# Optimization experiments

Measured on AMD Instinct MI355X. Metric: run time of the kernel, lower is better.

The kernel has to match this reference:

```python
import jax, jax.numpy as jnp
import numpy as np

BN_EPS = 1e-5
K = 3  # k_size


def _unfold(x, k):
    # torch F.unfold with padding=k//2, stride=1, viewed as (B, C, k*k, H, W).
    # Kernel positions are row-major (i slow, j fast), matching torch layout.
    p = k // 2
    B, C, H, W = x.shape
    xp = jnp.pad(x, ((0, 0), (0, 0), (p, p), (p, p)))
    pats = jnp.stack([xp[:, :, i:i + H, j:j + W]
                      for i in range(k) for j in range(k)], axis=2)
    return pats  # (B, C, k*k, H, W)


def _conv1x1(x, w, b):
    # w: (C_out, C_in), x: (B, C_in, H, W)
    return jnp.einsum('oc,bchw->bohw', w, x) + b[None, :, None, None]


def _bn(x, gamma, beta, mean, var):
    inv = gamma / jnp.sqrt(var + BN_EPS)
    return x * inv[None, :, None, None] + (beta - mean * inv)[None, :, None, None]


def setup_inputs() -> dict:
    key = jax.random.key(0)
    ks = jax.random.split(key, 12)
    B, C, H, W = 8, 256, 64, 64
    s = lambda k_, *sh: jax.random.normal(k_, sh, dtype=jnp.float32) * 0.05
    return {
        'x': jax.random.normal(ks[0], (B, C, H, W), dtype=jnp.float32),
        # feature_embedding: Conv2d(C, C, 1) + BN
        'w_embed': s(ks[1], C, C), 'b_embed': jnp.zeros((C,), jnp.float32),
        'bn1_gamma': jnp.ones((C,), jnp.float32), 'bn1_beta': jnp.zeros((C,), jnp.float32),
        'bn1_mean': jnp.zeros((C,), jnp.float32), 'bn1_var': jnp.ones((C,), jnp.float32),
        # enhance: Conv2d(2C, C, 1) + BN
        'w_enh': s(ks[2], C, 2 * C), 'b_enh': jnp.zeros((C,), jnp.float32),
        'bn2_gamma': jnp.ones((C,), jnp.float32), 'bn2_beta': jnp.zeros((C,), jnp.float32),
        'bn2_mean': jnp.zeros((C,), jnp.float32), 'bn2_var': jnp.ones((C,), jnp.float32),
        # weight_gen: Conv2d(2C, C//4, 1) -> ReLU -> Conv2d(C//4, C, 1) -> Sigmoid
        'w_g1': s(ks[3], C // 4, 2 * C), 'b_g1': jnp.zeros((C // 4,), jnp.float32),
        'w_g2': s(ks[4], C, C // 4), 'b_g2': jnp.zeros((C,), jnp.float32),
    }


def reference(x, w_embed, b_embed, bn1_gamma, bn1_beta, bn1_mean, bn1_var,
              w_enh, b_enh, bn2_gamma, bn2_beta, bn2_mean, bn2_var,
              w_g1, b_g1, w_g2, b_g2):
    B, C, H, W = x.shape
    # ---- feature embedding: 1x1 conv + BN (eval) + ReLU
    fe = jax.nn.relu(_bn(_conv1x1(x, w_embed, b_embed),
                         bn1_gamma, bn1_beta, bn1_mean, bn1_var))
    # ---- region similarity: cosine(center pixel, each kxk neighbor) over C
    pats = _unfold(fe, K)                       # (B, C, k2, H, W)
    sim = jnp.einsum('bchw,bckhw->bkhw', fe, pats)
    norm_c = jnp.sqrt(jnp.sum(fe * fe, axis=1))             # (B, H, W)
    norm_p = jnp.sqrt(jnp.sum(pats * pats, axis=1))         # (B, k2, H, W)
    sim = sim / (norm_c[:, None] * norm_p + 1e-7)
    sim = jax.nn.softmax(sim, axis=1)                       # over k2 window
    # ---- dynamic feature aggregation on original x
    xpats = _unfold(x, K)                                   # (B, C, k2, H, W)
    agg = jnp.einsum('bckhw,bkhw->bchw', xpats, sim)
    enhanced = jax.nn.relu(_bn(_conv1x1(jnp.concatenate([x, agg], axis=1), w_enh, b_enh),
                               bn2_gamma, bn2_beta, bn2_mean, bn2_var))
    # ---- output modulation (SE-style gating)
    pooled = jnp.mean(jnp.concatenate([x, enhanced], axis=1), axis=(2, 3), keepdims=True)
    h = jax.nn.relu(_conv1x1(pooled, w_g1, b_g1))
    weights = jax.nn.sigmoid(_conv1x1(h, w_g2, b_g2))       # (B, C, 1, 1)
    return x + weights * enhanced
```

## Files before the change

kernel.cpp:

```cpp
#include <hip/hip_runtime.h>
#include <math.h>

typedef unsigned short u16;
typedef unsigned int   u32;
typedef __attribute__((ext_vector_type(8))) short short8;
typedef __attribute__((ext_vector_type(4))) float f32x4;

#define OFS_XB   0ul
#define OFS_W1B  8388608ul
#define OFS_W2B  8421376ul
#define OFS_B1   8486912ul
#define OFS_B2   8487168ul
#define OFS_POOL 8487424ul
#define OFS_ENH  8491520ul

__device__ __forceinline__ u16 f2bf(float x) {
    union { float f; u32 u; } v; v.f = x;
    u32 r = v.u + 0x7fffu + ((v.u >> 16) & 1u);
    return (u16)(r >> 16);
}
__device__ __forceinline__ float bf2f(u16 h) {
    union { u32 u; float f; } v; v.u = ((u32)h) << 16;
    return v.f;
}
__device__ __forceinline__ void ld_g2l_16(u16* l, const u16* g) {
    __builtin_amdgcn_global_load_lds(
        (const __attribute__((address_space(1))) u32*)g,
        (__attribute__((address_space(3))) u32*)l,
        16, 0, 0);
}

__global__ __launch_bounds__(256) void k_cvt(
    const float* __restrict__ x, u16* __restrict__ xb, float* __restrict__ pool,
    const float* __restrict__ w1, const float* __restrict__ b1,
    const float* __restrict__ g1, const float* __restrict__ be1,
    const float* __restrict__ m1, const float* __restrict__ v1,
    const float* __restrict__ w2, const float* __restrict__ b2,
    const float* __restrict__ g2, const float* __restrict__ be2,
    const float* __restrict__ m2, const float* __restrict__ v2,
    u16* __restrict__ w1b, u16* __restrict__ w2b,
    float* __restrict__ b1f, float* __restrict__ b2f)
{
    __shared__ float tile[64][65];
    const int t = threadIdx.x;
    const int id = blockIdx.x;
    if (id < 1) {
        const float4 z = {0.f, 0.f, 0.f, 0.f};
#pragma unroll
        for (int i = 0; i < 4; ++i) ((float4*)pool)[i * 256 + t] = z;
        return;
    }
    if (id < 771) {
        int idx = (id - 1) * 256 + t;
        if (idx < 65536) {
            int o = idx >> 8;
            float inv = g1[o] * rsqrtf(v1[o] + 1e-5f);
            w1b[idx] = f2bf(w1[idx] * inv);
        } else if (idx < 196608) {
            int j = idx - 65536;
            int o = j >> 9;
            float inv = g2[o] * rsqrtf(v2[o] + 1e-5f);
            w2b[j] = f2bf(w2[j] * inv);
        } else if (idx < 196864) {
            int o = idx - 196608;
            float inv = g1[o] * rsqrtf(v1[o] + 1e-5f);
            b1f[o] = b1[o] * inv + be1[o] - m1[o] * inv;
        } else if (idx < 197120) {
            int o = idx - 196864;
            float inv = g2[o] * rsqrtf(v2[o] + 1e-5f);
            b2f[o] = b2[o] * inv + be2[o] - m2[o] * inv;
        }
        return;
    }
    const int cid = id - 771;
    const int pt = cid & 63, ct = (cid >> 6) & 3, b = cid >> 8;
    const float* src = x + (((size_t)(b * 256 + ct * 64)) << 12) + pt * 64;
#pragma unroll
    for (int i = 0; i < 16; ++i) {
        int idx = i * 256 + t;
        int cl = idx >> 6, pl = idx & 63;
        tile[cl][pl] = src[((size_t)cl << 12) + pl];
    }
    __syncthreads();
#pragma unroll
    for (int i = 0; i < 8; ++i) {
        int idx = i * 256 + t;
        int pl = idx >> 5, c2 = idx & 31;
        int cl = c2 * 2;
        u32 lo = f2bf(tile[cl][pl]);
        u32 hi = f2bf(tile[cl + 1][pl]);
        *(u32*)(xb + (((size_t)(b * 4096 + pt * 64 + pl)) << 9) + ct * 64 + cl) = lo | (hi << 16);
    }
    if (t < 64) {
        float s = 0.f;
#pragma unroll
        for (int i = 0; i < 64; ++i) s += tile[t][i];
        atomicAdd(&pool[(b << 9) + ct * 64 + t], s * (1.f / 4096.f));
    }
}

template<int KIN, bool OUTBF, bool DOPOOL>
__global__ __launch_bounds__(256) void k_gemm(
    const u16* __restrict__ xb, const u16* __restrict__ Wb,
    const float* __restrict__ biasf, void* __restrict__ outp,
    float* __restrict__ poolp)
{
    __shared__ __align__(16) u16 Wl[4096];
    __shared__ __align__(16) u16 Xl[4096];
    __shared__ float sbias[128];
    const int t = threadIdx.x;
    const int lane = t & 63;
    const int wv = t >> 6;
    const int id = blockIdx.x;
    const int p_blk = (((id >> 4) << 3) | (id & 7)) * 128;
    const int o_blk = ((id >> 3) & 1) * 128;
    const int owg = (wv & 1) * 4;
    const int pwg = (wv >> 1) * 4;
    const int r16 = lane & 15, q = lane >> 4;
    if (t < 128) sbias[t] = biasf[o_blk + t];

    f32x4 acc[4][4];
#pragma unroll
    for (int i = 0; i < 4; ++i)
#pragma unroll
        for (int j = 0; j < 4; ++j) acc[i][j] = (f32x4){0.f, 0.f, 0.f, 0.f};

    for (int kc = 0; kc < KIN / 32; ++kc) {
        const int kk = kc * 32 + q * 8;
#pragma unroll
        for (int s = 0; s < 4; ++s) {
            const int bi = wv * 4 + s;
            const u16* g;
            u16* l;
            if (bi < 8) {
                g = Wb + (size_t)(o_blk + bi * 16 + r16) * KIN + kk;
                l = Wl + bi * 512;
            } else {
                g = xb + (((size_t)(p_blk + (bi - 8) * 16 + r16)) << 9) + kk;
                l = Xl + (bi - 8) * 512;
            }
            ld_g2l_16(l, g);
        }
        __syncthreads();
        short8 af[4], bf[4];
#pragma unroll
        for (int i = 0; i < 4; ++i) af[i] = *(const short8*)(Wl + (owg + i) * 512 + lane * 8);
#pragma unroll
        for (int j = 0; j < 4; ++j) bf[j] = *(const short8*)(Xl + (pwg + j) * 512 + lane * 8);
#pragma unroll
        for (int i = 0; i < 4; ++i)
#pragma unroll
            for (int j = 0; j < 4; ++j)
                acc[i][j] = __builtin_amdgcn_mfma_f32_16x16x32_bf16(af[i], bf[j], acc[i][j], 0, 0, 0);
        __syncthreads();
    }

    float bia[4][4];
#pragma unroll
    for (int i = 0; i < 4; ++i)
#pragma unroll
        for (int r = 0; r < 4; ++r) bia[i][r] = sbias[owg * 16 + i * 16 + q * 4 + r];
    const int bidx = p_blk >> 12;
    const int pin0 = (p_blk & 4095) + pwg * 16 + r16;
#pragma unroll
    for (int i = 0; i < 4; ++i) {
#pragma unroll
        for (int r = 0; r < 4; ++r) {
            const int o = o_blk + owg * 16 + i * 16 + q * 4 + r;
            const size_t rowb = ((size_t)(bidx * 256 + o)) << 12;
            float ps = 0.f;
#pragma unroll
            for (int j = 0; j < 4; ++j) {
                float v = fmaxf(acc[i][j][r] + bia[i][r], 0.f);
                const size_t oi = rowb + pin0 + j * 16;
                ((u16*)outp)[oi] = f2bf(v);
                ps += v;
            }
            if (DOPOOL) {
                ps += __shfl_down(ps, 8, 16);
                ps += __shfl_down(ps, 4, 16);
                ps += __shfl_down(ps, 2, 16);
                ps += __shfl_down(ps, 1, 16);
                if (r16 == 0)
                    atomicAdd(&poolp[(bidx << 9) + 256 + o], ps * (1.f / 4096.f));
            }
        }
    }
}

__global__ __launch_bounds__(512) void k_simagg(
    const u16* __restrict__ fe, const u16* __restrict__ xb, u16* __restrict__ xbo)
{
    __shared__ __align__(16) u16 st[3 * 16384];
    __shared__ float red[8][64][13];
    __shared__ float ws9[9][64];
    const int t = threadIdx.x;
    const int id = blockIdx.x;
    const int b = id & 7, h = id >> 3;
    const int rows[3] = {h > 0 ? h - 1 : 0, h, h < 63 ? h + 1 : 63};

    {
        const u16* base = fe + ((size_t)(b * 256) << 12);
#pragma unroll
        for (int it = 0; it < 12; ++it) {
            const int flat = it * 512 + t;
            const int r = flat >> 11, j = flat & 2047;
            const u16* gs = base + ((size_t)(j >> 3) << 12) + rows[r] * 64 + (j & 7) * 8;
            ld_g2l_16(st + r * 16384 + j * 8, gs);
        }
    }
    __syncthreads();
    const int w = t & 63, sl = t >> 6;
    {
        const int wl = w > 0 ? w - 1 : 0, wr = w < 63 ? w + 1 : 63;
        float dot[9] = {};
        float nn[3] = {};
        const u16* s0 = st + sl * 2048;
#pragma unroll 4
        for (int ci = 0; ci < 32; ++ci) {
            const u16* pc = s0 + ci * 64;
            float v[9];
#pragma unroll
            for (int r = 0; r < 3; ++r) {
                v[r * 3 + 0] = bf2f(pc[r * 16384 + wl]);
                v[r * 3 + 1] = bf2f(pc[r * 16384 + w]);
                v[r * 3 + 2] = bf2f(pc[r * 16384 + wr]);
            }
            const float c0 = v[4];
#pragma unroll
            for (int k = 0; k < 9; ++k) dot[k] = fmaf(c0, v[k], dot[k]);
#pragma unroll
            for (int r = 0; r < 3; ++r) nn[r] = fmaf(v[r * 3 + 1], v[r * 3 + 1], nn[r]);
        }
#pragma unroll
        for (int k = 0; k < 9; ++k) red[sl][w][k] = dot[k];
#pragma unroll
        for (int r = 0; r < 3; ++r) red[sl][w][9 + r] = nn[r];
    }
    __syncthreads();
    {
        const u16* base = xb + ((size_t)(b * 4096) << 9);
#pragma unroll
        for (int it = 0; it < 12; ++it) {
            const int flat = it * 512 + t;
            const int r = flat >> 11, j = flat & 2047;
            const u16* gs = base + (((size_t)(rows[r] * 64 + (j >> 5))) << 9) + (j & 31) * 8;
            ld_g2l_16(st + r * 16384 + j * 8, gs);
        }
    }
    if (t < 64) {
        float dk[9], nr[3];
#pragma unroll
        for (int k = 0; k < 9; ++k) {
            float s = red[0][w][k];
#pragma unroll
            for (int g = 1; g < 8; ++g) s += red[g][w][k];
            dk[k] = s;
        }
#pragma unroll
        for (int r = 0; r < 3; ++r) {
            float s = red[0][w][9 + r];
#pragma unroll
            for (int g = 1; g < 8; ++g) s += red[g][w][9 + r];
            nr[r] = s;
        }
        const float nc = sqrtf(nr[1]);
        float sv[9], mk[9];
#pragma unroll
        for (int di = -1; di <= 1; ++di) {
#pragma unroll
            for (int dj = -1; dj <= 1; ++dj) {
                const int k = (di + 1) * 3 + (dj + 1);
                const int hn = h + di, wn = w + dj;
                const float mask = (hn >= 0 && hn < 64 && wn >= 0 && wn < 64) ? 1.f : 0.f;
                const int wc = wn < 0 ? 0 : (wn > 63 ? 63 : wn);
                const float nk = __shfl(nr[di + 1], wc, 64);
                mk[k] = mask;
                sv[k] = mask * dk[k] / (nc * sqrtf(nk) + 1e-7f);
            }
        }
        float mx = sv[0];
#pragma unroll
        for (int k = 1; k < 9; ++k) mx = fmaxf(mx, sv[k]);
        float e[9], sum = 0.f;
#pragma unroll
        for (int k = 0; k < 9; ++k) { e[k] = expf(sv[k] - mx); sum += e[k]; }
        const float rs = 1.f / sum;
#pragma unroll
        for (int k = 0; k < 9; ++k) ws9[k][w] = mk[k] * e[k] * rs;
    }
    __syncthreads();
    const int cpair = (t & 127) * 2;
    const int pxg = t >> 7;
    u16* orow = xbo + (((size_t)(b * 4096 + h * 64)) << 9) + 256 + cpair;
#pragma unroll 4
    for (int pi = 0; pi < 16; ++pi) {
        const int px = pxg * 16 + pi;
        const int pL = px > 0 ? px - 1 : 0, pR = px < 63 ? px + 1 : 63;
        const int pxs[3] = {pL, px, pR};
        float m9[9];
#pragma unroll
        for (int k = 0; k < 9; ++k) m9[k] = ws9[k][px];
        float a0 = 0.f, a1 = 0.f;
#pragma unroll
        for (int r = 0; r < 3; ++r)
#pragma unroll
            for (int j = 0; j < 3; ++j) {
                const u32 vv = *(const u32*)(st + r * 16384 + pxs[j] * 256 + cpair);
                a0 = fmaf(bf2f((u16)(vv & 0xffffu)), m9[r * 3 + j], a0);
                a1 = fmaf(bf2f((u16)(vv >> 16)),     m9[r * 3 + j], a1);
            }
        *(u32*)(orow + ((size_t)px << 9)) = (u32)f2bf(a0) | ((u32)f2bf(a1) << 16);
    }
}

__global__ __launch_bounds__(256) void k_final(
    const u16* __restrict__ xb, const u16* __restrict__ enh,
    const float* __restrict__ pool,
    const float* __restrict__ wg1, const float* __restrict__ bg1,
    const float* __restrict__ wg2, const float* __restrict__ bg2,
    float* __restrict__ out)
{
    __shared__ float pl[512];
    __shared__ float hpart[4][64];
    __shared__ float hb[64];
    __shared__ float sg[256];
    const int t = threadIdx.x;
    const int id = blockIdx.x;
    const int b = id & 7, rg = id >> 3;
    pl[t] = pool[b * 512 + t];
    pl[t + 256] = pool[b * 512 + 256 + t];
    __syncthreads();
    {
        const int o = t & 63, seg = t >> 6;
        float s = 0.f;
        const float* wr_ = wg1 + o * 512 + seg * 128;
        const float* pr_ = pl + seg * 128;
#pragma unroll 4
        for (int j = 0; j < 128; ++j) s = fmaf(wr_[j], pr_[j], s);
        hpart[seg][o] = s;
    }
    __syncthreads();
    if (t < 64)
        hb[t] = fmaxf(hpart[0][t] + hpart[1][t] + hpart[2][t] + hpart[3][t] + bg1[t], 0.f);
    __syncthreads();
    {
        float s2 = bg2[t];
        const float* w2 = wg2 + t * 64;
#pragma unroll 4
        for (int j = 0; j < 64; ++j) s2 = fmaf(w2[j], hb[j], s2);
        sg[t] = 1.f / (1.f + expf(-s2));
    }
    __syncthreads();
    const int w = t & 63, cs = t >> 6;
    const int p = rg * 64 + w;
    const u16* xrow = xb + (((size_t)(b * 4096 + p)) << 9) + cs * 64;
#pragma unroll 2
    for (int cc = 0; cc < 8; ++cc) {
        short8 xv = *(const short8*)(xrow + cc * 8);
#pragma unroll
        for (int u = 0; u < 8; ++u) {
            const int c = cs * 64 + cc * 8 + u;
            const float gt = sg[c];
            const size_t off = (((size_t)(b * 256 + c)) << 12) + p;
            out[off] = fmaf(gt, bf2f(enh[off]), bf2f((u16)xv[u]));
        }
    }
}

extern "C" void kernel_launch(void* const* d_in, const int* in_sizes, int n_in,
                              void* d_out, int out_size, void* d_ws, size_t ws_size,
                              hipStream_t stream)
{
    const float* x       = (const float*)d_in[0];
    const float* w_embed = (const float*)d_in[1];
    const float* b_embed = (const float*)d_in[2];
    const float* g1      = (const float*)d_in[3];
    const float* be1     = (const float*)d_in[4];
    const float* m1      = (const float*)d_in[5];
    const float* v1      = (const float*)d_in[6];
    const float* w_enh   = (const float*)d_in[7];
    const float* b_enh   = (const float*)d_in[8];
    const float* g2      = (const float*)d_in[9];
    const float* be2     = (const float*)d_in[10];
    const float* m2      = (const float*)d_in[11];
    const float* v2      = (const float*)d_in[12];
    const float* w_g1    = (const float*)d_in[13];
    const float* b_g1    = (const float*)d_in[14];
    const float* w_g2    = (const float*)d_in[15];
    const float* b_g2    = (const float*)d_in[16];
    float* ws  = (float*)d_ws;
    float* out = (float*)d_out;

    u16*   xb   = (u16*)(ws + OFS_XB);
    u16*   w1b  = (u16*)(ws + OFS_W1B);
    u16*   w2b  = (u16*)(ws + OFS_W2B);
    float* b1f  = ws + OFS_B1;
    float* b2f  = ws + OFS_B2;
    float* pool = ws + OFS_POOL;
    u16*   enh  = (u16*)(ws + OFS_ENH);
    u16*   fe   = (u16*)d_out;

    k_cvt<<<dim3(2819), dim3(256), 0, stream>>>(
        x, xb, pool,
        w_embed, b_embed, g1, be1, m1, v1,
        w_enh, b_enh, g2, be2, m2, v2, w1b, w2b, b1f, b2f);
    k_gemm<256, true, false><<<dim3(512), dim3(256), 0, stream>>>(xb, w1b, b1f, (void*)fe, nullptr);
    k_simagg<<<dim3(512), dim3(512), 0, stream>>>(fe, xb, xb);
    k_gemm<512, true, true><<<dim3(512), dim3(256), 0, stream>>>(xb, w2b, b2f, (void*)enh, pool);
    k_final<<<dim3(512), dim3(256), 0, stream>>>(xb, enh, pool, w_g1, b_g1, w_g2, b_g2, out);
}
```

Measured before the change: 205.1 us.

## Store fe pixel-major with swizzled LDS, vectorize simagg and final epilogue

The first GEMM now writes the feature embedding transposed to pixel-major (channel-contiguous) through a swizzled LDS staging buffer. The similarity kernel then reads channel vectors with 16-byte LDS loads and computes each neighbor dot product over a channel slice, reusing the center dot as its norm. The aggregation uses 4-wide loads, and the final kernel reads x in fp32 along channel rows with vectorized float4 loads and stores instead of strided scalar accesses. This trades extra LDS in the GEMM epilogue and an added fp32 read of x for coalesced, vectorized memory traffic.

```diff
diff --git a/kernel.cpp b/kernel.cpp
--- a/kernel.cpp
+++ b/kernel.cpp
@@ -4,6 +4,7 @@
 typedef unsigned short u16;
 typedef unsigned int   u32;
 typedef __attribute__((ext_vector_type(8))) short short8;
+typedef __attribute__((ext_vector_type(4))) short s16x4;
 typedef __attribute__((ext_vector_type(4))) float f32x4;
 
 #define OFS_XB   0ul
@@ -99,7 +100,7 @@
     }
 }
 
-template<int KIN, bool OUTBF, bool DOPOOL>
+template<int KIN, bool OUTT, bool DOPOOL>
 __global__ __launch_bounds__(256) void k_gemm(
     const u16* __restrict__ xb, const u16* __restrict__ Wb,
     const float* __restrict__ biasf, void* __restrict__ outp,
@@ -107,6 +108,7 @@
 {
     __shared__ __align__(16) u16 Wl[4096];
     __shared__ __align__(16) u16 Xl[4096];
+    __shared__ __align__(16) u16 ct[OUTT ? 16384 : 4];
     __shared__ float sbias[128];
     const int t = threadIdx.x;
     const int lane = t & 63;
@@ -161,6 +163,36 @@
 #pragma unroll
         for (int r = 0; r < 4; ++r) bia[i][r] = sbias[owg * 16 + i * 16 + q * 4 + r];
     const int bidx = p_blk >> 12;
+
+    if (OUTT) {
+#pragma unroll
+        for (int i = 0; i < 4; ++i) {
+#pragma unroll
+            for (int j = 0; j < 4; ++j) {
+                const int px_l = pwg * 16 + j * 16 + r16;
+#pragma unroll
+                for (int rp = 0; rp < 2; ++rp) {
+                    const int r0 = rp * 2;
+                    const int o_l = owg * 16 + i * 16 + q * 4 + r0;
+                    const float v0 = fmaxf(acc[i][j][r0] + bia[i][r0], 0.f);
+                    const float v1 = fmaxf(acc[i][j][r0 + 1] + bia[i][r0 + 1], 0.f);
+                    const u32 pk = (u32)f2bf(v0) | ((u32)f2bf(v1) << 16);
+                    *(u32*)((char*)ct + px_l * 256 + ((o_l * 2) ^ ((px_l & 7) << 4))) = pk;
+                }
+            }
+        }
+        __syncthreads();
+        u16* feT = (u16*)outp;
+#pragma unroll
+        for (int it = 0; it < 16; ++it) {
+            const int idx = it * 256 + t;
+            const int px_l = idx >> 5, cd = idx & 31;
+            s16x4 v = *(const s16x4*)((char*)ct + px_l * 256 + ((cd * 8) ^ ((px_l & 7) << 4)));
+            *(s16x4*)(feT + (((size_t)(bidx * 4096 + (p_blk & 4095) + px_l)) << 8) + o_blk + cd * 4) = v;
+        }
+        return;
+    }
+
     const int pin0 = (p_blk & 4095) + pwg * 16 + r16;
 #pragma unroll
     for (int i = 0; i < 4; ++i) {
@@ -199,57 +231,76 @@
     const int b = id & 7, h = id >> 3;
     const int rows[3] = {h > 0 ? h - 1 : 0, h, h < 63 ? h + 1 : 63};
 
-    {
-        const u16* base = fe + ((size_t)(b * 256) << 12);
-#pragma unroll
-        for (int it = 0; it < 12; ++it) {
-            const int flat = it * 512 + t;
-            const int r = flat >> 11, j = flat & 2047;
-            const u16* gs = base + ((size_t)(j >> 3) << 12) + rows[r] * 64 + (j & 7) * 8;
-            ld_g2l_16(st + r * 16384 + j * 8, gs);
-        }
+#pragma unroll
+    for (int it = 0; it < 12; ++it) {
+        const int flat = it * 512 + t;
+        const int r = flat >> 11, j = flat & 2047;
+        const int px = j >> 5, cs = j & 31;
+        const u16* gs = fe + (((size_t)(b * 4096 + rows[r] * 64 + px)) << 8) + ((cs ^ (px & 7)) << 3);
+        ld_g2l_16(st + r * 16384 + j * 8, gs);
     }
     __syncthreads();
     const int w = t & 63, sl = t >> 6;
     {
-        const int wl = w > 0 ? w - 1 : 0, wr = w < 63 ? w + 1 : 63;
-        float dot[9] = {};
-        float nn[3] = {};
-        const u16* s0 = st + sl * 2048;
-#pragma unroll 4
-        for (int ci = 0; ci < 32; ++ci) {
-            const u16* pc = s0 + ci * 64;
-            float v[9];
-#pragma unroll
-            for (int r = 0; r < 3; ++r) {
-                v[r * 3 + 0] = bf2f(pc[r * 16384 + wl]);
-                v[r * 3 + 1] = bf2f(pc[r * 16384 + w]);
-                v[r * 3 + 2] = bf2f(pc[r * 16384 + wr]);
-            }
-            const float c0 = v[4];
-#pragma unroll
-            for (int k = 0; k < 9; ++k) dot[k] = fmaf(c0, v[k], dot[k]);
-#pragma unroll
-            for (int r = 0; r < 3; ++r) nn[r] = fmaf(v[r * 3 + 1], v[r * 3 + 1], nn[r]);
+        float cvec[32];
+        float dot[9];
+        float nn0 = 0.f, nn2 = 0.f;
+        const int c0 = sl * 4;
+        {
+            const u16* rowp = st + 16384 + w * 256;
+            float s = 0.f;
+#pragma unroll
+            for (int i = 0; i < 4; ++i) {
+                short8 v = *(const short8*)(rowp + (((c0 + i) ^ (w & 7)) << 3));
+#pragma unroll
+                for (int u = 0; u < 8; ++u) {
+                    float f = bf2f((u16)v[u]);
+                    cvec[i * 8 + u] = f;
+                    s = fmaf(f, f, s);
+                }
+            }
+            dot[4] = s;
+        }
+#pragma unroll
+        for (int r = 0; r < 3; ++r) {
+#pragma unroll
+            for (int dj = -1; dj <= 1; ++dj) {
+                if (r == 1 && dj == 0) continue;
+                const int k = r * 3 + dj + 1;
+                const int wn = w + dj;
+                const int pxn = wn < 0 ? 0 : (wn > 63 ? 63 : wn);
+                const u16* rowp = st + r * 16384 + pxn * 256;
+                float s = 0.f, qq = 0.f;
+#pragma unroll
+                for (int i = 0; i < 4; ++i) {
+                    short8 v = *(const short8*)(rowp + (((c0 + i) ^ (pxn & 7)) << 3));
+#pragma unroll
+                    for (int u = 0; u < 8; ++u) {
+                        float f = bf2f((u16)v[u]);
+                        s = fmaf(cvec[i * 8 + u], f, s);
+                        if (dj == 0) qq = fmaf(f, f, qq);
+                    }
+                }
+                dot[k] = s;
+                if (dj == 0) { if (r == 0) nn0 = qq; else nn2 = qq; }
+            }
         }
 #pragma unroll
         for (int k = 0; k < 9; ++k) red[sl][w][k] = dot[k];
-#pragma unroll
-        for (int r = 0; r < 3; ++r) red[sl][w][9 + r] = nn[r];
-    }
-    __syncthreads();
-    {
-        const u16* base = xb + ((size_t)(b * 4096) << 9);
-#pragma unroll
-        for (int it = 0; it < 12; ++it) {
-            const int flat = it * 512 + t;
-            const int r = flat >> 11, j = flat & 2047;
-            const u16* gs = base + (((size_t)(rows[r] * 64 + (j >> 5))) << 9) + (j & 31) * 8;
-            ld_g2l_16(st + r * 16384 + j * 8, gs);
-        }
+        red[sl][w][9] = nn0;
+        red[sl][w][10] = nn2;
+    }
+    __syncthreads();
+#pragma unroll
+    for (int it = 0; it < 12; ++it) {
+        const int flat = it * 512 + t;
+        const int r = flat >> 11, j = flat & 2047;
+        const int px = j >> 5, cs = j & 31;
+        const u16* gs = xb + (((size_t)(b * 4096 + rows[r] * 64 + px)) << 9) + ((cs ^ (px & 7)) << 3);
+        ld_g2l_16(st + r * 16384 + j * 8, gs);
     }
     if (t < 64) {
-        float dk[9], nr[3];
+        float dk[9];
 #pragma unroll
         for (int k = 0; k < 9; ++k) {
             float s = red[0][w][k];
@@ -257,14 +308,11 @@
             for (int g = 1; g < 8; ++g) s += red[g][w][k];
             dk[k] = s;
         }
-#pragma unroll
-        for (int r = 0; r < 3; ++r) {
-            float s = red[0][w][9 + r];
-#pragma unroll
-            for (int g = 1; g < 8; ++g) s += red[g][w][9 + r];
-            nr[r] = s;
-        }
-        const float nc = sqrtf(nr[1]);
+        float nr0 = red[0][w][9], nr2 = red[0][w][10];
+#pragma unroll
+        for (int g = 1; g < 8; ++g) { nr0 += red[g][w][9]; nr2 += red[g][w][10]; }
+        float nr[3] = {nr0, dk[4], nr2};
+        const float nc = sqrtf(dk[4]);
         float sv[9], mk[9];
 #pragma unroll
         for (int di = -1; di <= 1; ++di) {
@@ -290,32 +338,38 @@
         for (int k = 0; k < 9; ++k) ws9[k][w] = mk[k] * e[k] * rs;
     }
     __syncthreads();
-    const int cpair = (t & 127) * 2;
-    const int pxg = t >> 7;
-    u16* orow = xbo + (((size_t)(b * 4096 + h * 64)) << 9) + 256 + cpair;
-#pragma unroll 4
-    for (int pi = 0; pi < 16; ++pi) {
-        const int px = pxg * 16 + pi;
+    const int cd = t & 63, pxg = t >> 6;
+    u16* orow = xbo + (((size_t)(b * 4096 + h * 64)) << 9) + 256 + cd * 4;
+#pragma unroll
+    for (int pi = 0; pi < 8; ++pi) {
+        const int px = pxg * 8 + pi;
         const int pL = px > 0 ? px - 1 : 0, pR = px < 63 ? px + 1 : 63;
         const int pxs[3] = {pL, px, pR};
-        float m9[9];
-#pragma unroll
-        for (int k = 0; k < 9; ++k) m9[k] = ws9[k][px];
-        float a0 = 0.f, a1 = 0.f;
-#pragma unroll
-        for (int r = 0; r < 3; ++r)
+        float a0 = 0.f, a1 = 0.f, a2 = 0.f, a3 = 0.f;
+#pragma unroll
+        for (int r = 0; r < 3; ++r) {
 #pragma unroll
             for (int j = 0; j < 3; ++j) {
-                const u32 vv = *(const u32*)(st + r * 16384 + pxs[j] * 256 + cpair);
-                a0 = fmaf(bf2f((u16)(vv & 0xffffu)), m9[r * 3 + j], a0);
-                a1 = fmaf(bf2f((u16)(vv >> 16)),     m9[r * 3 + j], a1);
-            }
-        *(u32*)(orow + ((size_t)px << 9)) = (u32)f2bf(a0) | ((u32)f2bf(a1) << 16);
+                const float m = ws9[r * 3 + j][px];
+                const int pp = pxs[j];
+                const u16* pB = st + r * 16384 + pp * 256 +
+                                ((((cd >> 1) ^ (pp & 7)) << 3) | ((cd & 1) << 2));
+                s16x4 v = *(const s16x4*)pB;
+                a0 = fmaf(bf2f((u16)v[0]), m, a0);
+                a1 = fmaf(bf2f((u16)v[1]), m, a1);
+                a2 = fmaf(bf2f((u16)v[2]), m, a2);
+                a3 = fmaf(bf2f((u16)v[3]), m, a3);
+            }
+        }
+        s16x4 sv4;
+        sv4[0] = (short)f2bf(a0); sv4[1] = (short)f2bf(a1);
+        sv4[2] = (short)f2bf(a2); sv4[3] = (short)f2bf(a3);
+        *(s16x4*)(orow + ((size_t)px << 9)) = sv4;
     }
 }
 
 __global__ __launch_bounds__(256) void k_final(
-    const u16* __restrict__ xb, const u16* __restrict__ enh,
+    const float* __restrict__ x, const u16* __restrict__ enh,
     const float* __restrict__ pool,
     const float* __restrict__ wg1, const float* __restrict__ bg1,
     const float* __restrict__ wg2, const float* __restrict__ bg2,
@@ -327,7 +381,7 @@
     __shared__ float sg[256];
     const int t = threadIdx.x;
     const int id = blockIdx.x;
-    const int b = id & 7, rg = id >> 3;
+    const int b = id & 7, cg = id >> 3;
     pl[t] = pool[b * 512 + t];
     pl[t + 256] = pool[b * 512 + 256 + t];
     __syncthreads();
@@ -352,19 +406,29 @@
         sg[t] = 1.f / (1.f + expf(-s2));
     }
     __syncthreads();
-    const int w = t & 63, cs = t >> 6;
-    const int p = rg * 64 + w;
-    const u16* xrow = xb + (((size_t)(b * 4096 + p)) << 9) + cs * 64;
-#pragma unroll 2
-    for (int cc = 0; cc < 8; ++cc) {
-        short8 xv = *(const short8*)(xrow + cc * 8);
-#pragma unroll
-        for (int u = 0; u < 8; ++u) {
-            const int c = cs * 64 + cc * 8 + u;
-            const float gt = sg[c];
-            const size_t off = (((size_t)(b * 256 + c)) << 12) + p;
-            out[off] = fmaf(gt, bf2f(enh[off]), bf2f((u16)xv[u]));
-        }
+    const int cl = t >> 6, l = t & 63;
+    const int c = cg * 4 + cl;
+    const float gt = sg[c];
+    const float* xp = x + (((size_t)(b * 256 + c)) << 12);
+    const u16*   ep = enh + (((size_t)(b * 256 + c)) << 12);
+    float*       op = out + (((size_t)(b * 256 + c)) << 12);
+#pragma unroll
+    for (int ch = 0; ch < 8; ++ch) {
+        const int base = ch * 512 + l * 8;
+        short8 ev = *(const short8*)(ep + base);
+        float4 x0 = *(const float4*)(xp + base);
+        float4 x1 = *(const float4*)(xp + base + 4);
+        float4 o0, o1;
+        o0.x = fmaf(gt, bf2f((u16)ev[0]), x0.x);
+        o0.y = fmaf(gt, bf2f((u16)ev[1]), x0.y);
+        o0.z = fmaf(gt, bf2f((u16)ev[2]), x0.z);
+        o0.w = fmaf(gt, bf2f((u16)ev[3]), x0.w);
+        o1.x = fmaf(gt, bf2f((u16)ev[4]), x1.x);
+        o1.y = fmaf(gt, bf2f((u16)ev[5]), x1.y);
+        o1.z = fmaf(gt, bf2f((u16)ev[6]), x1.z);
+        o1.w = fmaf(gt, bf2f((u16)ev[7]), x1.w);
+        *(float4*)(op + base) = o0;
+        *(float4*)(op + base + 4) = o1;
     }
 }
 
@@ -407,6 +471,6 @@
         w_enh, b_enh, g2, be2, m2, v2, w1b, w2b, b1f, b2f);
     k_gemm<256, true, false><<<dim3(512), dim3(256), 0, stream>>>(xb, w1b, b1f, (void*)fe, nullptr);
     k_simagg<<<dim3(512), dim3(512), 0, stream>>>(fe, xb, xb);
-    k_gemm<512, true, true><<<dim3(512), dim3(256), 0, stream>>>(xb, w2b, b2f, (void*)enh, pool);
-    k_final<<<dim3(512), dim3(256), 0, stream>>>(xb, enh, pool, w_g1, b_g1, w_g2, b_g2, out);
-}
+    k_gemm<512, false, true><<<dim3(512), dim3(256), 0, stream>>>(xb, w2b, b2f, (void*)enh, pool);
+    k_final<<<dim3(512), dim3(256), 0, stream>>>(x, enh, pool, w_g1, b_g1, w_g2, b_g2, out);
+}
```

Measured after the change: 206.2 us. No clear change (+0.5%).
